# Performance work log

Measured on AMD Instinct MI355X. Metric: run time of the kernel, lower is better.

## Reference

```python
import jax, jax.numpy as jnp
import numpy as np
from jax import lax

E, H, TOPK = 32, 512, 4
B, S = 2, 1024

def setup_inputs() -> dict:
    key = jax.random.key(0)
    ks = jax.random.split(key, 5)
    scale = 0.05
    return {
        "x": jax.random.normal(ks[0], (B, S, H), dtype=jnp.float32),
        "gate_w": jax.random.normal(ks[1], (E, H), dtype=jnp.float32) * scale,
        "w_gate": jax.random.normal(ks[2], (E, 2 * H, H), dtype=jnp.float32) * scale,
        "w_up": jax.random.normal(ks[3], (E, 2 * H, H), dtype=jnp.float32) * scale,
        "w_down": jax.random.normal(ks[4], (E, H, 2 * H), dtype=jnp.float32) * scale,
        "top_k": TOPK,
    }

def reference(x, gate_w, w_gate, w_up, w_down, top_k):
    b, s, h = x.shape
    n = b * s
    e = gate_w.shape[0]
    xf = x.reshape(n, h)                                   # [N,H]
    logits = xf @ gate_w.T                                 # [N,E]
    probs = jax.nn.softmax(logits, axis=-1)
    w, sel = lax.top_k(probs, top_k)                       # [N,K]
    w = w / jnp.sum(w, axis=-1, keepdims=True)
    # per-(token,expert) combine weight; zero for unselected experts
    comb = jnp.zeros((n, e), dtype=x.dtype).at[
        jnp.arange(n)[:, None], sel].add(w)                # [N,E]

    def body(acc, ws):
        wg, wu, wd, ce = ws                                # [2H,H],[2H,H],[H,2H],[N]
        hidden = jax.nn.silu(xf @ wg.T) * (xf @ wu.T)      # [N,2H]
        out = hidden @ wd.T                                # [N,H]
        return acc + out * ce[:, None], None

    acc0 = jnp.zeros_like(xf)
    acc, _ = lax.scan(body, acc0, (w_gate, w_up, w_down, comb.T))
    return acc.reshape(b, s, h)
```

## Files before the change

kernel.cpp:

```cpp
#include <hip/hip_runtime.h>
#include <hip/hip_bf16.h>
#include <math.h>

#define NE 32
#define H 512
#define H2 1024
#define NTOK 2048
#define CAP 2048
#define BM 64
#define MAXT64 160
#define TSTRIDE 144
#define CSTR 32
#define CVTB 1536

typedef __attribute__((ext_vector_type(8))) short bf16x8;
typedef __attribute__((ext_vector_type(4))) float f32x4;
typedef unsigned int uint;
typedef unsigned short ushort;

__device__ __forceinline__ uint bf16r(float f) {
    uint u = __float_as_uint(f);
    return (u + 0x7FFFu + ((u >> 16) & 1u)) >> 16;
}
__device__ __forceinline__ uint pack_bf16(float a, float b) {
    return bf16r(a) | (bf16r(b) << 16);
}
__device__ __forceinline__ float bf16f(ushort u) {
    return __uint_as_float(((uint)u) << 16);
}

__device__ __forceinline__ void dma16(const void* g, void* l) {
    __builtin_amdgcn_global_load_lds(
        (const __attribute__((address_space(1))) uint*)g,
        (__attribute__((address_space(3))) uint*)l, 16, 0, 0);
}

__device__ __forceinline__ void cvt_mat(const float* __restrict__ src,
                                        ushort* __restrict__ dst,
                                        int tg, int nt, int nch)
{
    for (int c = tg; c < nch; c += nt) {
        const float4* s = (const float4*)src + (size_t)c * 2;
        float4 x0 = s[0], x1 = s[1];
        uint4 v;
        v.x = pack_bf16(x0.x, x0.y); v.y = pack_bf16(x0.z, x0.w);
        v.z = pack_bf16(x1.x, x1.y); v.w = pack_bf16(x1.z, x1.w);
        ((uint4*)dst)[c] = v;
    }
}

__global__ __launch_bounds__(256) void prep_kernel(
    const float* __restrict__ x, const float* __restrict__ gate_w,
    int* __restrict__ cnt, int* __restrict__ listTok, int* __restrict__ listPair,
    float* __restrict__ listW, ushort* __restrict__ xbf,
    const float* __restrict__ wg, const float* __restrict__ wu,
    const float* __restrict__ wd,
    ushort* __restrict__ wgb, ushort* __restrict__ wub, ushort* __restrict__ wdb)
{
    const int b = blockIdx.x;
    if (b >= 512) {
        const int tg = (b - 512) * 256 + (int)threadIdx.x;
        const int nt = CVTB * 256;
        const int nch = NE * H2 * H / 8;
        cvt_mat(wg, wgb, tg, nt, nch);
        cvt_mat(wu, wub, tg, nt, nch);
        cvt_mat(wd, wdb, tg, nt, nch);
        return;
    }

    const int wave = threadIdx.x >> 6;
    const int lane = threadIdx.x & 63;
    const int t = b * 4 + wave;
    const int e = lane & 31;
    const int half = lane >> 5;

    const float4* xr = (const float4*)(x + (size_t)t * H + half * 256);
    const float4* gr = (const float4*)(gate_w + (size_t)e * H + half * 256);
    float acc = 0.f;
#pragma unroll 8
    for (int i = 0; i < 64; ++i) {
        float4 a = xr[i], g = gr[i];
        acc += a.x * g.x + a.y * g.y + a.z * g.z + a.w * g.w;
    }
    acc += __shfl_xor(acc, 32);

    float mx = acc;
#pragma unroll
    for (int m = 16; m >= 1; m >>= 1) mx = fmaxf(mx, __shfl_xor(mx, m));
    float p = __expf(acc - mx);
    float s = p;
#pragma unroll
    for (int m = 16; m >= 1; m >>= 1) s += __shfl_xor(s, m);
    float prob = p / s;

    int selk[4]; float wk[4]; float sum4 = 0.f;
#pragma unroll
    for (int k = 0; k < 4; ++k) {
        float v = prob; int idx = e;
#pragma unroll
        for (int m = 16; m >= 1; m >>= 1) {
            float v2 = __shfl_xor(v, m);
            int   i2 = __shfl_xor(idx, m);
            if (v2 > v || (v2 == v && i2 < idx)) { v = v2; idx = i2; }
        }
        selk[k] = idx; wk[k] = v; sum4 += v;
        if (e == idx) prob = -1.f;
    }

    if (lane < 4) {
        const int k = lane;
        const int ex = selk[k];
        const int pos = atomicAdd(&cnt[ex * CSTR], 1);
        listTok [ex * CAP + pos] = t;
        listPair[ex * CAP + pos] = t * 4 + k;
        listW   [ex * CAP + pos] = wk[k] / sum4;
    }

    const float4* xrow4 = (const float4*)(x + (size_t)t * H);
    float4 a0 = xrow4[lane * 2];
    float4 a1 = xrow4[lane * 2 + 1];
    uint4 o;
    o.x = pack_bf16(a0.x, a0.y); o.y = pack_bf16(a0.z, a0.w);
    o.z = pack_bf16(a1.x, a1.y); o.w = pack_bf16(a1.z, a1.w);
    ((uint4*)(xbf + (size_t)t * H))[lane] = o;
}

__global__ void sched_kernel(const int* __restrict__ cnt,
                             int* __restrict__ ntiles, int* __restrict__ desc)
{
    const int lane = threadIdx.x;
    int t = 0;
    if (lane < NE) t = (cnt[lane * CSTR] + 63) >> 6;
    int pre = t;
#pragma unroll
    for (int m = 1; m < 64; m <<= 1) {
        int v = __shfl_up(pre, m);
        if (lane >= m) pre += v;
    }
    const int off = pre - t;
    if (lane < NE)
        for (int i = 0; i < t; ++i) desc[off + i] = (lane << 16) | i;
    if (lane == 63) *ntiles = pre;
}

template<bool WB>
__global__ __launch_bounds__(256, 4) void moe_gemm1(
    const void* __restrict__ wgate_, const void* __restrict__ wup_,
    const ushort* __restrict__ xbf, const int* __restrict__ cnt,
    const int* __restrict__ listTok, const int* __restrict__ listPair,
    const float* __restrict__ listW, ushort* __restrict__ hidden,
    const int* __restrict__ ntiles, const int* __restrict__ desc)
{
    const int item = blockIdx.x;
    if (item >= (*ntiles) * 8) return;
    const int d  = desc[item >> 3];
    const int ch = item & 7;
    const int e  = d >> 16;
    const int mt = d & 0xffff;
    const int count = cnt[e * CSTR];
    const int m0 = mt * BM;

    __shared__ ushort smem[2 * 128 * 64];
    ushort* Gs = smem;
    ushort* Us = smem + 128 * 64;

    const int tid  = threadIdx.x;
    const int lane = tid & 63;
    const int w    = tid >> 6;
    const int l15  = lane & 15;
    const int quad = lane >> 4;

    const int arow = m0 + w * 16 + l15;
    const int atok = (arow < count) ? listTok[e * CAP + arow] : 0;
    const char* aptr = (const char*)(xbf + (size_t)atok * H);

    const int rr = lane >> 3;
    const int p  = lane & 7;
    const char* gsrc = nullptr; const char* usrc = nullptr;
    const int sr = tid >> 1;
    const int sh = tid & 1;
    const float* gF = nullptr; const float* uF = nullptr;
    if (WB) {
        const ushort* wgp = (const ushort*)wgate_;
        const ushort* wup = (const ushort*)wup_;
        const size_t rowi = (size_t)e * H2 + (size_t)(ch * 128 + w * 32 + rr);
        gsrc = (const char*)(wgp + rowi * H) + ((p ^ rr) << 4);
        usrc = (const char*)(wup + rowi * H) + ((p ^ rr) << 4);
    } else {
        gF = (const float*)wgate_ + ((size_t)e * H2 + (size_t)(ch * 128 + sr)) * H;
        uF = (const float*)wup_   + ((size_t)e * H2 + (size_t)(ch * 128 + sr)) * H;
    }

    f32x4 accg[8], accu[8];
    const f32x4 fz = {0.f, 0.f, 0.f, 0.f};
#pragma unroll
    for (int ni = 0; ni < 8; ++ni) { accg[ni] = fz; accu[ni] = fz; }

    uint4 a0 = *(const uint4*)(aptr + quad * 16);
    uint4 a1 = *(const uint4*)(aptr + 64 + quad * 16);

    for (int it = 0; it < 8; ++it) {
        __syncthreads();
        if (WB) {
#pragma unroll
            for (int i = 0; i < 4; ++i) {
                dma16(gsrc + i * (8 * H * 2), (char*)Gs + w * 4096 + i * 1024);
                dma16(usrc + i * (8 * H * 2), (char*)Us + w * 4096 + i * 1024);
            }
        } else {
#pragma unroll
            for (int i = 0; i < 4; ++i) {
                const int pslot = sh * 4 + i;
                const int pc = pslot ^ (sr & 7);
                const float4* s1 = (const float4*)(gF + it * 64 + pc * 8);
                float4 g0 = s1[0], g1 = s1[1];
                uint4 v;
                v.x = pack_bf16(g0.x, g0.y); v.y = pack_bf16(g0.z, g0.w);
                v.z = pack_bf16(g1.x, g1.y); v.w = pack_bf16(g1.z, g1.w);
                ((uint4*)Gs)[sr * 8 + pslot] = v;
                const float4* s2 = (const float4*)(uF + it * 64 + pc * 8);
                float4 u0 = s2[0], u1 = s2[1];
                uint4 q;
                q.x = pack_bf16(u0.x, u0.y); q.y = pack_bf16(u0.z, u0.w);
                q.z = pack_bf16(u1.x, u1.y); q.w = pack_bf16(u1.z, u1.w);
                ((uint4*)Us)[sr * 8 + pslot] = q;
            }
        }
        const int itn = (it < 7) ? it + 1 : 7;
        uint4 an0 = *(const uint4*)(aptr + itn * 128 + quad * 16);
        uint4 an1 = *(const uint4*)(aptr + itn * 128 + 64 + quad * 16);
        __syncthreads();

#pragma unroll
        for (int ks = 0; ks < 2; ++ks) {
            bf16x8 af = ks ? *(bf16x8*)&a1 : *(bf16x8*)&a0;
#pragma unroll
            for (int ni = 0; ni < 8; ++ni) {
                const int n = ni * 16 + l15;
                const int slot = n * 8 + ((ks * 4 + quad) ^ (n & 7));
                bf16x8 bg = ((const bf16x8*)Gs)[slot];
                bf16x8 bu = ((const bf16x8*)Us)[slot];
                accg[ni] = __builtin_amdgcn_mfma_f32_16x16x32_bf16(af, bg, accg[ni], 0, 0, 0);
                accu[ni] = __builtin_amdgcn_mfma_f32_16x16x32_bf16(af, bu, accu[ni], 0, 0, 0);
            }
        }
        a0 = an0; a1 = an1;
        if (WB) { gsrc += 128; usrc += 128; }
    }

    __syncthreads();
    ushort* T = smem;
#pragma unroll
    for (int r = 0; r < 4; ++r) {
        const int row = w * 16 + quad * 4 + r;
        const int slot2 = m0 + row;
        const float wgt = (slot2 < count) ? listW[e * CAP + slot2] : 0.f;
#pragma unroll
        for (int ni = 0; ni < 8; ++ni) {
            float gv = accg[ni][r], uv = accu[ni][r];
            float hv = (gv / (1.f + __expf(-gv))) * uv * wgt;
            T[row * TSTRIDE + ni * 16 + l15] = (ushort)bf16r(hv);
        }
    }
    __syncthreads();
    {
        const int row = tid >> 2;
        const int qp  = tid & 3;
        const int slot2 = m0 + row;
        if (slot2 < count) {
            const int pr = listPair[e * CAP + slot2];
            uint4* dst = (uint4*)(hidden + (size_t)pr * H2 + ch * 128) + qp * 4;
            const uint4* src = (const uint4*)(T + row * TSTRIDE) + qp * 4;
#pragma unroll
            for (int i = 0; i < 4; ++i) dst[i] = src[i];
        }
    }
}

template<bool WB>
__global__ __launch_bounds__(256, 4) void moe_gemm2(
    const void* __restrict__ wdown_, const ushort* __restrict__ hidden,
    const int* __restrict__ cnt, const int* __restrict__ listPair,
    ushort* __restrict__ pairOut,
    const int* __restrict__ ntiles, const int* __restrict__ desc)
{
    const int item = blockIdx.x;
    if (item >= (*ntiles) * 8) return;
    const int d   = desc[item >> 3];
    const int ks2 = (item >> 2) & 1;
    const int ch  = item & 3;
    const int e   = d >> 16;
    const int mt  = d & 0xffff;
    const int count = cnt[e * CSTR];
    const int m0 = mt * BM;

    __shared__ ushort smem[9216];
    ushort* Bs = smem;

    const int tid  = threadIdx.x;
    const int lane = tid & 63;
    const int w    = tid >> 6;
    const int l15  = lane & 15;
    const int quad = lane >> 4;

    const int arow = m0 + w * 16 + l15;
    const int apr  = (arow < count) ? listPair[e * CAP + arow] : 0;
    const char* aptr = (const char*)(hidden + (size_t)apr * H2 + ks2 * 512);

    const int rr = lane >> 3;
    const int p  = lane & 7;
    const char* bsrc = nullptr;
    const int sr = tid >> 1;
    const int sh = tid & 1;
    const float* bF = nullptr;
    if (WB) {
        const ushort* wdp = (const ushort*)wdown_;
        const size_t rowi = (size_t)e * H + (size_t)(ch * 128 + w * 32 + rr);
        bsrc = (const char*)(wdp + rowi * H2 + ks2 * 512) + ((p ^ rr) << 4);
    } else {
        bF = (const float*)wdown_ + ((size_t)e * H + (size_t)(ch * 128 + sr)) * H2 + ks2 * 512;
    }

    f32x4 acc[8];
    const f32x4 fz = {0.f, 0.f, 0.f, 0.f};
#pragma unroll
    for (int ni = 0; ni < 8; ++ni) acc[ni] = fz;

    uint4 a0 = *(const uint4*)(aptr + quad * 16);
    uint4 a1 = *(const uint4*)(aptr + 64 + quad * 16);

    for (int it = 0; it < 8; ++it) {
        __syncthreads();
        if (WB) {
#pragma unroll
            for (int i = 0; i < 4; ++i)
                dma16(bsrc + i * (8 * H2 * 2), (char*)Bs + w * 4096 + i * 1024);
        } else {
#pragma unroll
            for (int i = 0; i < 4; ++i) {
                const int pslot = sh * 4 + i;
                const int pc = pslot ^ (sr & 7);
                const float4* s1 = (const float4*)(bF + it * 64 + pc * 8);
                float4 b0 = s1[0], b1 = s1[1];
                uint4 v;
                v.x = pack_bf16(b0.x, b0.y); v.y = pack_bf16(b0.z, b0.w);
                v.z = pack_bf16(b1.x, b1.y); v.w = pack_bf16(b1.z, b1.w);
                ((uint4*)Bs)[sr * 8 + pslot] = v;
            }
        }
        const int itn = (it < 7) ? it + 1 : 7;
        uint4 an0 = *(const uint4*)(aptr + itn * 128 + quad * 16);
        uint4 an1 = *(const uint4*)(aptr + itn * 128 + 64 + quad * 16);
        __syncthreads();

#pragma unroll
        for (int ks = 0; ks < 2; ++ks) {
            bf16x8 af = ks ? *(bf16x8*)&a1 : *(bf16x8*)&a0;
#pragma unroll
            for (int ni = 0; ni < 8; ++ni) {
                const int n = ni * 16 + l15;
                const int slot = n * 8 + ((ks * 4 + quad) ^ (n & 7));
                bf16x8 bb = ((const bf16x8*)Bs)[slot];
                acc[ni] = __builtin_amdgcn_mfma_f32_16x16x32_bf16(af, bb, acc[ni], 0, 0, 0);
            }
        }
        a0 = an0; a1 = an1;
        if (WB) bsrc += 128;
    }

    __syncthreads();
    ushort* T = smem;
#pragma unroll
    for (int r = 0; r < 4; ++r) {
        const int row = w * 16 + quad * 4 + r;
#pragma unroll
        for (int ni = 0; ni < 8; ++ni)
            T[row * TSTRIDE + ni * 16 + l15] = (ushort)bf16r(acc[ni][r]);
    }
    __syncthreads();
    {
        const int row = tid >> 2;
        const int qp  = tid & 3;
        const int slot2 = m0 + row;
        if (slot2 < count) {
            const int pr = listPair[e * CAP + slot2];
            uint4* dst = (uint4*)(pairOut + ((size_t)(ks2 << 13) + pr) * H + ch * 128) + qp * 4;
            const uint4* src = (const uint4*)(T + row * TSTRIDE) + qp * 4;
#pragma unroll
            for (int i = 0; i < 4; ++i) dst[i] = src[i];
        }
    }
}

__global__ __launch_bounds__(256) void combine_kernel(
    const ushort* __restrict__ pairOut, float* __restrict__ out)
{
    const int tok = blockIdx.x * 4 + (threadIdx.x >> 6);
    const int c   = (threadIdx.x & 63) * 8;
    float s[8];
#pragma unroll
    for (int i = 0; i < 8; ++i) s[i] = 0.f;
#pragma unroll
    for (int j = 0; j < 8; ++j) {
        const int row = ((j >> 2) << 13) + tok * 4 + (j & 3);
        uint4 v = *(const uint4*)(pairOut + (size_t)row * H + c);
        const ushort* u = (const ushort*)&v;
#pragma unroll
        for (int i = 0; i < 8; ++i) s[i] += bf16f(u[i]);
    }
    float4* o = (float4*)(out + (size_t)tok * H + c);
    o[0] = make_float4(s[0], s[1], s[2], s[3]);
    o[1] = make_float4(s[4], s[5], s[6], s[7]);
}

extern "C" void kernel_launch(void* const* d_in, const int* in_sizes, int n_in,
                              void* d_out, int out_size, void* d_ws, size_t ws_size,
                              hipStream_t stream)
{
    (void)in_sizes; (void)n_in; (void)out_size;
    const float* x      = (const float*)d_in[0];
    const float* gate_w = (const float*)d_in[1];
    const float* w_gate = (const float*)d_in[2];
    const float* w_up   = (const float*)d_in[3];
    const float* w_down = (const float*)d_in[4];

    char* ws = (char*)d_ws;
    int* cnt    = (int*)ws;
    int* ntiles = (int*)(ws + 4096);
    int* desc   = (int*)(ws + 4224);

    size_t off = 8192;
    int*    listTok  = (int*)(ws + off);   off += (size_t)NE * CAP * 4;
    int*    listPair = (int*)(ws + off);   off += (size_t)NE * CAP * 4;
    float*  listW    = (float*)(ws + off); off += (size_t)NE * CAP * 4;
    ushort* xbf      = (ushort*)(ws + off); off += (size_t)NTOK * H * 2;
    ushort* hidden   = (ushort*)(ws + off); off += (size_t)NTOK * 4 * H2 * 2;
    ushort* pairOut  = (ushort*)(ws + off); off += (size_t)2 * NTOK * 4 * H * 2;
    ushort* wgb = (ushort*)(ws + off); off += (size_t)NE * H2 * H * 2;
    ushort* wub = (ushort*)(ws + off); off += (size_t)NE * H2 * H * 2;
    ushort* wdb = (ushort*)(ws + off); off += (size_t)NE * H * H2 * 2;
    const size_t need_full = off;

    const bool full = (ws_size >= need_full);

    hipMemsetAsync(ws, 0, 4352, stream);

    if (full) {
        prep_kernel<<<512 + CVTB, 256, 0, stream>>>(
            x, gate_w, cnt, listTok, listPair, listW, xbf,
            w_gate, w_up, w_down, wgb, wub, wdb);
        sched_kernel<<<1, 64, 0, stream>>>(cnt, ntiles, desc);
        moe_gemm1<true><<<MAXT64 * 8, 256, 0, stream>>>(
            (const void*)wgb, (const void*)wub, xbf, cnt, listTok, listPair,
            listW, hidden, ntiles, desc);
        moe_gemm2<true><<<MAXT64 * 8, 256, 0, stream>>>(
            (const void*)wdb, hidden, cnt, listPair, pairOut, ntiles, desc);
    } else {
        prep_kernel<<<512, 256, 0, stream>>>(
            x, gate_w, cnt, listTok, listPair, listW, xbf,
            w_gate, w_up, w_down, nullptr, nullptr, nullptr);
        sched_kernel<<<1, 64, 0, stream>>>(cnt, ntiles, desc);
        moe_gemm1<false><<<MAXT64 * 8, 256, 0, stream>>>(
            (const void*)w_gate, (const void*)w_up, xbf, cnt, listTok, listPair,
            listW, hidden, ntiles, desc);
        moe_gemm2<false><<<MAXT64 * 8, 256, 0, stream>>>(
            (const void*)w_down, hidden, cnt, listPair, pairOut, ntiles, desc);
    }
    combine_kernel<<<NTOK / 4, 256, 0, stream>>>(pairOut, (float*)d_out);
}
```

Before: 298.2 us.

## Split gate and weight conversion kernels, overlap down-proj conversion with GEMM1

The fused prep kernel is split into a gating kernel and a separate fp32-to-bf16 weight conversion kernel for w_gate and w_up. The conversion uses nontemporal loads, and the number of conversion blocks is raised. The gating kernel now stages gate_w in XOR-swizzled shared memory instead of reading it from global per lane. The w_down conversion is moved into extra blocks appended to the GEMM1 grid, so it can overlap GEMM1 compute instead of preceding it. The cost is extra launches and conversion blocks that compete with GEMM1 tiles for CUs.

```diff
diff --git a/kernel.cpp b/kernel.cpp
--- a/kernel.cpp
+++ b/kernel.cpp
@@ -11,7 +11,8 @@
 #define MAXT64 160
 #define TSTRIDE 144
 #define CSTR 32
-#define CVTB 1536
+#define CVTB 2048
+#define WDTB 512
 
 typedef __attribute__((ext_vector_type(8))) short bf16x8;
 typedef __attribute__((ext_vector_type(4))) float f32x4;
@@ -40,8 +41,9 @@
                                         int tg, int nt, int nch)
 {
     for (int c = tg; c < nch; c += nt) {
-        const float4* s = (const float4*)src + (size_t)c * 2;
-        float4 x0 = s[0], x1 = s[1];
+        const f32x4* s = (const f32x4*)src + (size_t)c * 2;
+        f32x4 x0 = __builtin_nontemporal_load(s);
+        f32x4 x1 = __builtin_nontemporal_load(s + 1);
         uint4 v;
         v.x = pack_bf16(x0.x, x0.y); v.y = pack_bf16(x0.z, x0.w);
         v.z = pack_bf16(x1.x, x1.y); v.w = pack_bf16(x1.z, x1.w);
@@ -49,37 +51,34 @@
     }
 }
 
-__global__ __launch_bounds__(256) void prep_kernel(
+__global__ __launch_bounds__(256) void gate_kernel(
     const float* __restrict__ x, const float* __restrict__ gate_w,
     int* __restrict__ cnt, int* __restrict__ listTok, int* __restrict__ listPair,
-    float* __restrict__ listW, ushort* __restrict__ xbf,
-    const float* __restrict__ wg, const float* __restrict__ wu,
-    const float* __restrict__ wd,
-    ushort* __restrict__ wgb, ushort* __restrict__ wub, ushort* __restrict__ wdb)
-{
+    float* __restrict__ listW, ushort* __restrict__ xbf)
+{
+    __shared__ float4 gws[4096];
+    const int tid = threadIdx.x;
+    for (int i = tid; i < 4096; i += 256) {
+        const int r = i >> 7, pp = i & 127;
+        gws[(r << 7) | (pp ^ (r & 7))] = ((const float4*)gate_w)[i];
+    }
+
     const int b = blockIdx.x;
-    if (b >= 512) {
-        const int tg = (b - 512) * 256 + (int)threadIdx.x;
-        const int nt = CVTB * 256;
-        const int nch = NE * H2 * H / 8;
-        cvt_mat(wg, wgb, tg, nt, nch);
-        cvt_mat(wu, wub, tg, nt, nch);
-        cvt_mat(wd, wdb, tg, nt, nch);
-        return;
-    }
-
-    const int wave = threadIdx.x >> 6;
-    const int lane = threadIdx.x & 63;
+    const int wave = tid >> 6;
+    const int lane = tid & 63;
     const int t = b * 4 + wave;
     const int e = lane & 31;
     const int half = lane >> 5;
 
     const float4* xr = (const float4*)(x + (size_t)t * H + half * 256);
-    const float4* gr = (const float4*)(gate_w + (size_t)e * H + half * 256);
+    __syncthreads();
+
     float acc = 0.f;
 #pragma unroll 8
     for (int i = 0; i < 64; ++i) {
-        float4 a = xr[i], g = gr[i];
+        const int p = half * 64 + i;
+        float4 a = xr[i];
+        float4 g = gws[(e << 7) | (p ^ (e & 7))];
         acc += a.x * g.x + a.y * g.y + a.z * g.z + a.w * g.w;
     }
     acc += __shfl_xor(acc, 32);
@@ -125,6 +124,17 @@
     ((uint4*)(xbf + (size_t)t * H))[lane] = o;
 }
 
+__global__ __launch_bounds__(256) void cvt_kernel(
+    const float* __restrict__ wg, const float* __restrict__ wu,
+    ushort* __restrict__ wgb, ushort* __restrict__ wub)
+{
+    const int tg = blockIdx.x * 256 + (int)threadIdx.x;
+    const int nt = CVTB * 256;
+    const int nch = NE * H2 * H / 8;
+    cvt_mat(wg, wgb, tg, nt, nch);
+    cvt_mat(wu, wub, tg, nt, nch);
+}
+
 __global__ void sched_kernel(const int* __restrict__ cnt,
                              int* __restrict__ ntiles, int* __restrict__ desc)
 {
@@ -149,9 +159,15 @@
     const ushort* __restrict__ xbf, const int* __restrict__ cnt,
     const int* __restrict__ listTok, const int* __restrict__ listPair,
     const float* __restrict__ listW, ushort* __restrict__ hidden,
-    const int* __restrict__ ntiles, const int* __restrict__ desc)
+    const int* __restrict__ ntiles, const int* __restrict__ desc,
+    const float* __restrict__ wdF, ushort* __restrict__ wdb_)
 {
     const int item = blockIdx.x;
+    if (WB && item >= MAXT64 * 8) {
+        const int tg = (item - MAXT64 * 8) * 256 + (int)threadIdx.x;
+        cvt_mat(wdF, wdb_, tg, WDTB * 256, NE * H * H2 / 8);
+        return;
+    }
     if (item >= (*ntiles) * 8) return;
     const int d  = desc[item >> 3];
     const int ch = item & 7;
@@ -446,23 +462,22 @@
     hipMemsetAsync(ws, 0, 4352, stream);
 
     if (full) {
-        prep_kernel<<<512 + CVTB, 256, 0, stream>>>(
-            x, gate_w, cnt, listTok, listPair, listW, xbf,
-            w_gate, w_up, w_down, wgb, wub, wdb);
+        gate_kernel<<<512, 256, 0, stream>>>(
+            x, gate_w, cnt, listTok, listPair, listW, xbf);
+        cvt_kernel<<<CVTB, 256, 0, stream>>>(w_gate, w_up, wgb, wub);
         sched_kernel<<<1, 64, 0, stream>>>(cnt, ntiles, desc);
-        moe_gemm1<true><<<MAXT64 * 8, 256, 0, stream>>>(
+        moe_gemm1<true><<<MAXT64 * 8 + WDTB, 256, 0, stream>>>(
             (const void*)wgb, (const void*)wub, xbf, cnt, listTok, listPair,
-            listW, hidden, ntiles, desc);
+            listW, hidden, ntiles, desc, w_down, wdb);
         moe_gemm2<true><<<MAXT64 * 8, 256, 0, stream>>>(
             (const void*)wdb, hidden, cnt, listPair, pairOut, ntiles, desc);
     } else {
-        prep_kernel<<<512, 256, 0, stream>>>(
-            x, gate_w, cnt, listTok, listPair, listW, xbf,
-            w_gate, w_up, w_down, nullptr, nullptr, nullptr);
+        gate_kernel<<<512, 256, 0, stream>>>(
+            x, gate_w, cnt, listTok, listPair, listW, xbf);
         sched_kernel<<<1, 64, 0, stream>>>(cnt, ntiles, desc);
         moe_gemm1<false><<<MAXT64 * 8, 256, 0, stream>>>(
             (const void*)w_gate, (const void*)w_up, xbf, cnt, listTok, listPair,
-            listW, hidden, ntiles, desc);
+            listW, hidden, ntiles, desc, nullptr, nullptr);
         moe_gemm2<false><<<MAXT64 * 8, 256, 0, stream>>>(
             (const void*)w_down, hidden, cnt, listPair, pairOut, ntiles, desc);
     }
```

New measurement: 282.0 us. 1.06x faster.

## Move w_down bf16 conversion into gemm1 launch and use nontemporal loads

Applied to the files above, without the earlier changes.

The fp32-to-bf16 conversion of w_down moves out of the prep kernel. It now runs in 512 extra blocks at the front of the gemm1 grid, so it overlaps with the gate/up GEMM instead of lengthening prep. The prep conversion grid grows from 1536 to 2048 blocks. The weight loads become nontemporal so they stream without polluting the cache. The overlap depends on block scheduling order, and the conversion blocks compete with GEMM blocks for CUs.

```diff
diff --git a/kernel.cpp b/kernel.cpp
--- a/kernel.cpp
+++ b/kernel.cpp
@@ -11,7 +11,8 @@
 #define MAXT64 160
 #define TSTRIDE 144
 #define CSTR 32
-#define CVTB 1536
+#define CVTB 2048
+#define WDTB 512
 
 typedef __attribute__((ext_vector_type(8))) short bf16x8;
 typedef __attribute__((ext_vector_type(4))) float f32x4;
@@ -40,8 +41,9 @@
                                         int tg, int nt, int nch)
 {
     for (int c = tg; c < nch; c += nt) {
-        const float4* s = (const float4*)src + (size_t)c * 2;
-        float4 x0 = s[0], x1 = s[1];
+        const f32x4* s = (const f32x4*)src + (size_t)c * 2;
+        f32x4 x0 = __builtin_nontemporal_load(s);
+        f32x4 x1 = __builtin_nontemporal_load(s + 1);
         uint4 v;
         v.x = pack_bf16(x0.x, x0.y); v.y = pack_bf16(x0.z, x0.w);
         v.z = pack_bf16(x1.x, x1.y); v.w = pack_bf16(x1.z, x1.w);
@@ -54,8 +56,7 @@
     int* __restrict__ cnt, int* __restrict__ listTok, int* __restrict__ listPair,
     float* __restrict__ listW, ushort* __restrict__ xbf,
     const float* __restrict__ wg, const float* __restrict__ wu,
-    const float* __restrict__ wd,
-    ushort* __restrict__ wgb, ushort* __restrict__ wub, ushort* __restrict__ wdb)
+    ushort* __restrict__ wgb, ushort* __restrict__ wub)
 {
     const int b = blockIdx.x;
     if (b >= 512) {
@@ -64,7 +65,6 @@
         const int nch = NE * H2 * H / 8;
         cvt_mat(wg, wgb, tg, nt, nch);
         cvt_mat(wu, wub, tg, nt, nch);
-        cvt_mat(wd, wdb, tg, nt, nch);
         return;
     }
 
@@ -149,9 +149,18 @@
     const ushort* __restrict__ xbf, const int* __restrict__ cnt,
     const int* __restrict__ listTok, const int* __restrict__ listPair,
     const float* __restrict__ listW, ushort* __restrict__ hidden,
-    const int* __restrict__ ntiles, const int* __restrict__ desc)
-{
-    const int item = blockIdx.x;
+    const int* __restrict__ ntiles, const int* __restrict__ desc,
+    const float* __restrict__ wdF, ushort* __restrict__ wdb_)
+{
+    int item = blockIdx.x;
+    if (WB) {
+        if (item < WDTB) {
+            const int tg = item * 256 + (int)threadIdx.x;
+            cvt_mat(wdF, wdb_, tg, WDTB * 256, NE * H * H2 / 8);
+            return;
+        }
+        item -= WDTB;
+    }
     if (item >= (*ntiles) * 8) return;
     const int d  = desc[item >> 3];
     const int ch = item & 7;
@@ -448,21 +457,21 @@
     if (full) {
         prep_kernel<<<512 + CVTB, 256, 0, stream>>>(
             x, gate_w, cnt, listTok, listPair, listW, xbf,
-            w_gate, w_up, w_down, wgb, wub, wdb);
+            w_gate, w_up, wgb, wub);
         sched_kernel<<<1, 64, 0, stream>>>(cnt, ntiles, desc);
-        moe_gemm1<true><<<MAXT64 * 8, 256, 0, stream>>>(
+        moe_gemm1<true><<<WDTB + MAXT64 * 8, 256, 0, stream>>>(
             (const void*)wgb, (const void*)wub, xbf, cnt, listTok, listPair,
-            listW, hidden, ntiles, desc);
+            listW, hidden, ntiles, desc, w_down, wdb);
         moe_gemm2<true><<<MAXT64 * 8, 256, 0, stream>>>(
             (const void*)wdb, hidden, cnt, listPair, pairOut, ntiles, desc);
     } else {
         prep_kernel<<<512, 256, 0, stream>>>(
             x, gate_w, cnt, listTok, listPair, listW, xbf,
-            w_gate, w_up, w_down, nullptr, nullptr, nullptr);
+            nullptr, nullptr, nullptr, nullptr);
         sched_kernel<<<1, 64, 0, stream>>>(cnt, ntiles, desc);
         moe_gemm1<false><<<MAXT64 * 8, 256, 0, stream>>>(
             (const void*)w_gate, (const void*)w_up, xbf, cnt, listTok, listPair,
-            listW, hidden, ntiles, desc);
+            listW, hidden, ntiles, desc, nullptr, nullptr);
         moe_gemm2<false><<<MAXT64 * 8, 256, 0, stream>>>(
             (const void*)w_down, hidden, cnt, listPair, pairOut, ntiles, desc);
     }
```

Result: faster. 280.9 us (-5.8%).
